# Kernel optimization log

Hardware: AMD Instinct MI355X
Metric: run time of the kernel (lower is better)

## Reference

```python
import jax, jax.numpy as jnp
import numpy as np

BN_EPS = 1e-5

def _bn_eval(x, gamma, beta):
    # Fresh torch BatchNorm1d in eval mode: running_mean=0, running_var=1
    return x * (gamma / jnp.sqrt(1.0 + BN_EPS)) + beta

def setup_inputs() -> dict:
    key = jax.random.key(0)
    ks = jax.random.split(key, 10)
    Q, K, H, W, D = 64, 128, 24, 8, 128
    L = H * W            # seq_len = 192
    FF = 2048            # dim_feedforward
    q_feat = jax.random.normal(ks[0], (Q, H, W, D), dtype=jnp.float32)
    g_feat = jax.random.normal(ks[1], (K, H, W, D), dtype=jnp.float32)
    se = jax.random.normal(ks[2], (L, L), dtype=jnp.float32)
    score_embed = (se + se.T).reshape(1, 1, L, L)
    s = 1.0 / np.sqrt(D)
    fc0_w = jax.random.uniform(ks[3], (D, D), jnp.float32, -s, s)
    fc0_b = jax.random.uniform(ks[4], (D,), jnp.float32, -s, s)
    s2 = 1.0 / np.sqrt(L)
    fc2_w = jax.random.uniform(ks[5], (FF, L), jnp.float32, -s2, s2)
    fc2_b = jax.random.uniform(ks[6], (FF,), jnp.float32, -s2, s2)
    s3 = 1.0 / np.sqrt(FF)
    fc3_w = jax.random.uniform(ks[7], (1, FF), jnp.float32, -s3, s3)
    fc3_b = jax.random.uniform(ks[8], (1,), jnp.float32, -s3, s3)
    bn1_g = jnp.ones((1,)); bn1_b = jnp.zeros((1,))
    bn2_g = jnp.ones((FF,)) + 0.1 * jax.random.normal(ks[9], (FF,), jnp.float32)
    bn2_b = jnp.zeros((FF,))
    bn3_g = jnp.ones((1,)); bn3_b = jnp.zeros((1,))
    return dict(q_feat=q_feat, g_feat=g_feat, score_embed=score_embed,
                fc0_w=fc0_w, fc0_b=fc0_b, fc2_w=fc2_w, fc2_b=fc2_b,
                fc3_w=fc3_w, fc3_b=fc3_b, bn1_g=bn1_g, bn1_b=bn1_b,
                bn2_g=bn2_g, bn2_b=bn2_b, bn3_g=bn3_g, bn3_b=bn3_b)

def reference(q_feat, g_feat, score_embed, fc0_w, fc0_b, fc2_w, fc2_b,
              fc3_w, fc3_b, bn1_g, bn1_b, bn2_g, bn2_b, bn3_g, bn3_b):
    Q = q_feat.shape[0]
    K = g_feat.shape[0]
    D = q_feat.shape[-1]
    L = score_embed.shape[-1]  # seq_len
    tgt = q_feat.reshape(Q, L, D)
    mem = g_feat.reshape(K, L, D)
    query = tgt @ fc0_w.T + fc0_b      # [Q, L, D]
    key_ = mem @ fc0_w.T + fc0_b       # [K, L, D]
    # [Q, K, L(s), L(t)] score, modulated by broadcast sigmoid bias
    score = jnp.einsum('qtd,ksd->qkst', query, key_) * jax.nn.sigmoid(score_embed)
    score = score.reshape(Q * K, L, L)
    # max over s and over t, concatenated per pair -> [QK, 2L]
    score = jnp.concatenate([score.max(axis=1), score.max(axis=2)], axis=-1)
    score = score.reshape(-1, L)       # [2*QK, L]
    score = _bn_eval(score, bn1_g, bn1_b)
    score = score @ fc2_w.T + fc2_b    # [2*QK, FF]
    score = _bn_eval(score, bn2_g, bn2_b)
    score = jax.nn.relu(score)
    score = score @ fc3_w.T + fc3_b    # [2*QK, 1]
    score = score.reshape(-1, 2).sum(axis=-1, keepdims=True)  # [QK, 1]
    score = _bn_eval(score, bn3_g, bn3_b)
    return score.reshape(Q, K)
```

## Files before the change

### kernel.cpp

```cpp
#include <hip/hip_runtime.h>

#define LL 192
#define FF 2048

typedef __attribute__((__ext_vector_type__(8)))  __bf16 bf16x8;
typedef __attribute__((__ext_vector_type__(4)))  __bf16 bf16x4;
typedef __attribute__((__ext_vector_type__(4)))  float  f32x4;

#define MFMA16(a, b, c) __builtin_amdgcn_mfma_f32_16x16x32_bf16((a), (b), (c), 0, 0, 0)


__launch_bounds__(256, 2)
__global__ void proj_prep_kernel(const float* __restrict__ qf_in,
                                 const float* __restrict__ gf_in,
                                 const float* __restrict__ fc0w,
                                 const float* __restrict__ fc0b,
                                 const float* __restrict__ se,
                                 const float* __restrict__ fc2w,
                                 const float* __restrict__ fc2b,
                                 const float* __restrict__ bn2g,
                                 const float* __restrict__ bn2b,
                                 const float* __restrict__ fc3w,
                                 __bf16* __restrict__ kfragA,
                                 __bf16* __restrict__ qfrag16,
                                 float* __restrict__ sig32,
                                 __bf16* __restrict__ fc2w_bf,
                                 float* __restrict__ h2,
                                 float* __restrict__ bb2,
                                 float* __restrict__ f3)
{
    int bx = blockIdx.x, tid = threadIdx.x;
    if (bx >= 1152) {
        int i0 = (bx - 1152) * 256 + tid;
        const int stride = 160 * 256;
        const float c1 = rsqrtf(1.f + 1e-5f);
        for (int i = i0; i < LL * LL; i += stride) {
            int r = i & 3, lane = (i >> 2) & 63, tile = i >> 8;
            int jt = tile % 12, st = tile / 12;
            int s = st * 16 + (lane >> 4) * 4 + r;
            int t = jt * 16 + (lane & 15);
            sig32[i] = 1.f / (1.f + __expf(-se[s * 192 + t]));
        }
        for (int i = i0; i < FF * LL; i += stride)
            fc2w_bf[i] = (__bf16)fc2w[i];
        for (int i = i0; i < FF; i += stride) {
            float h = bn2g[i] * c1;
            h2[i]  = h;
            bb2[i] = fc2b[i] * h + bn2b[i];
            f3[i]  = fc3w[i];
        }
        return;
    }
    __shared__ __bf16 Xs[32][136];
    __shared__ __bf16 Ws[128][136];
    __shared__ __bf16 Os[4096];
    const float* src = (bx < 384) ? (qf_in + (size_t)bx * (32 * 128))
                                  : (gf_in + (size_t)(bx - 384) * (32 * 128));
#pragma unroll
    for (int it = 0; it < 4; ++it) {
        int e = (it * 256 + tid) * 4;
        int r = e >> 7, c = e & 127;
        float4 v = *reinterpret_cast<const float4*>(src + e);
        bf16x4 xv;
        xv[0] = (__bf16)v.x; xv[1] = (__bf16)v.y;
        xv[2] = (__bf16)v.z; xv[3] = (__bf16)v.w;
        *reinterpret_cast<bf16x4*>(&Xs[r][c]) = xv;
    }
#pragma unroll
    for (int it = 0; it < 16; ++it) {
        int e = (it * 256 + tid) * 4;
        int r = e >> 7, c = e & 127;
        float4 v = *reinterpret_cast<const float4*>(fc0w + e);
        bf16x4 xv;
        xv[0] = (__bf16)v.x; xv[1] = (__bf16)v.y;
        xv[2] = (__bf16)v.z; xv[3] = (__bf16)v.w;
        *reinterpret_cast<bf16x4*>(&Ws[r][c]) = xv;
    }
    __syncthreads();

    int wv = tid >> 6, lane = tid & 63, quad = lane >> 4, l16 = lane & 15;
    int n0 = wv * 32;
    f32x4 acc[2][2];
#pragma unroll
    for (int m = 0; m < 2; ++m)
#pragma unroll
        for (int n = 0; n < 2; ++n) acc[m][n] = (f32x4){0.f, 0.f, 0.f, 0.f};
#pragma unroll
    for (int ks = 0; ks < 4; ++ks) {
        bf16x8 a0 = *reinterpret_cast<const bf16x8*>(&Xs[l16][ks * 32 + quad * 8]);
        bf16x8 a1 = *reinterpret_cast<const bf16x8*>(&Xs[16 + l16][ks * 32 + quad * 8]);
        bf16x8 b0 = *reinterpret_cast<const bf16x8*>(&Ws[n0 + l16][ks * 32 + quad * 8]);
        bf16x8 b1 = *reinterpret_cast<const bf16x8*>(&Ws[n0 + 16 + l16][ks * 32 + quad * 8]);
        acc[0][0] = MFMA16(a0, b0, acc[0][0]);
        acc[0][1] = MFMA16(a0, b1, acc[0][1]);
        acc[1][0] = MFMA16(a1, b0, acc[1][0]);
        acc[1][1] = MFMA16(a1, b1, acc[1][1]);
    }
#pragma unroll
    for (int mt = 0; mt < 2; ++mt)
#pragma unroll
        for (int nt = 0; nt < 2; ++nt) {
            int d = n0 + nt * 16 + l16;
            float bv = fc0b[d];
            int abase = mt * 2048 + (d >> 5) * 512 + ((d >> 3) & 3) * 128 + (d & 7);
#pragma unroll
            for (int r = 0; r < 4; ++r)
                Os[abase + (quad * 4 + r) * 8] = (__bf16)(acc[mt][nt][r] + bv);
        }
    __syncthreads();

    int row0 = bx * 32;
    __bf16* dst;
    if (bx < 384) {
        int qi = row0 / 192, tg0 = (row0 % 192) >> 4;
        dst = qfrag16 + qi * 24576 + tg0 * 2048;
    } else {
        int rk0 = row0 - 12288;
        int ki = rk0 / 192, sg0 = (rk0 % 192) >> 4;
        dst = kfragA + ki * 24576 + sg0 * 2048;
    }
#pragma unroll
    for (int it = 0; it < 2; ++it) {
        int e = (it * 256 + tid) * 8;
        *reinterpret_cast<bf16x8*>(dst + e) =
            *reinterpret_cast<const bf16x8*>(&Os[e]);
    }
}

__launch_bounds__(256, 2)
__global__ void score_kernel(const __bf16* __restrict__ kfragA,
                             const __bf16* __restrict__ qfrag16,
                             const float* __restrict__ sig32,
                             const float* __restrict__ bn1g,
                             const float* __restrict__ bn1b,
                             __bf16* __restrict__ Sred)
{
    __shared__ __bf16 Abuf[8192];
    __shared__ __bf16 rowT4[16][200];

    int tid = threadIdx.x;
    int q = blockIdx.x & 63;
    int kbase = (blockIdx.x >> 6) << 2;
    int w = tid >> 6, lane = tid & 63, quad = lane >> 4, l16 = lane & 15;
    const float g1c = bn1g[0] * rsqrtf(1.f + 1e-5f);
    const float b1v = bn1b[0];

    bf16x8 Bf[3][4];
    {
        const __bf16* qb = qfrag16 + (size_t)q * 24576 + lane * 8;
#pragma unroll
        for (int j = 0; j < 3; ++j)
#pragma unroll
            for (int ks = 0; ks < 4; ++ks)
                Bf[j][ks] = *reinterpret_cast<const bf16x8*>(
                    qb + ((3 * w + j) * 4 + ks) * 512);
    }

#pragma unroll 1
    for (int kk = 0; kk < 4; ++kk) {
        int kidx = kbase + kk;
        const __bf16* kp = kfragA + (size_t)kidx * 24576;
        size_t ob = (size_t)(q * 128 + kidx) * 384;
        float cm0 = -3.0e38f, cm1 = -3.0e38f, cm2 = -3.0e38f;

#pragma unroll 1
        for (int h = 0; h < 3; ++h) {
#pragma unroll
            for (int it = 0; it < 4; ++it) {
                int e = (it * 256 + tid) * 8;
                *reinterpret_cast<bf16x8*>(&Abuf[e]) =
                    *reinterpret_cast<const bf16x8*>(kp + 8192 * h + e);
            }
            __syncthreads();

#pragma unroll 1
            for (int lsc = 0; lsc < 2; ++lsc) {
                f32x4 acc[2][3];
#pragma unroll
                for (int i = 0; i < 2; ++i)
#pragma unroll
                    for (int j = 0; j < 3; ++j)
                        acc[i][j] = (f32x4){0.f, 0.f, 0.f, 0.f};

#pragma unroll
                for (int ks = 0; ks < 4; ++ks) {
                    bf16x8 a0 = *reinterpret_cast<const bf16x8*>(
                        &Abuf[((lsc * 2 + 0) * 4 + ks) * 512 + lane * 8]);
                    bf16x8 a1 = *reinterpret_cast<const bf16x8*>(
                        &Abuf[((lsc * 2 + 1) * 4 + ks) * 512 + lane * 8]);
#pragma unroll
                    for (int j = 0; j < 3; ++j) {
                        acc[0][j] = MFMA16(a0, Bf[j][ks], acc[0][j]);
                        acc[1][j] = MFMA16(a1, Bf[j][ks], acc[1][j]);
                    }
                }

#pragma unroll
                for (int i = 0; i < 2; ++i) {
                    int stile = 4 * h + lsc * 2 + i;
                    const float* sp = sig32 +
                        ((size_t)(stile * 12 + 3 * w) * 64 + lane) * 4;
                    f32x4 s0 = *reinterpret_cast<const f32x4*>(sp);
                    f32x4 s1 = *reinterpret_cast<const f32x4*>(sp + 256);
                    f32x4 s2 = *reinterpret_cast<const f32x4*>(sp + 512);
                    float v00 = acc[i][0][0] * s0[0], v01 = acc[i][0][1] * s0[1];
                    float v02 = acc[i][0][2] * s0[2], v03 = acc[i][0][3] * s0[3];
                    float v10 = acc[i][1][0] * s1[0], v11 = acc[i][1][1] * s1[1];
                    float v12 = acc[i][1][2] * s1[2], v13 = acc[i][1][3] * s1[3];
                    float v20 = acc[i][2][0] * s2[0], v21 = acc[i][2][1] * s2[1];
                    float v22 = acc[i][2][2] * s2[2], v23 = acc[i][2][3] * s2[3];
                    float rm0 = fmaxf(fmaxf(v00, v10), v20);
                    float rm1 = fmaxf(fmaxf(v01, v11), v21);
                    float rm2 = fmaxf(fmaxf(v02, v12), v22);
                    float rm3 = fmaxf(fmaxf(v03, v13), v23);
                    cm0 = fmaxf(cm0, fmaxf(fmaxf(fmaxf(v00, v01), v02), v03));
                    cm1 = fmaxf(cm1, fmaxf(fmaxf(fmaxf(v10, v11), v12), v13));
                    cm2 = fmaxf(cm2, fmaxf(fmaxf(fmaxf(v20, v21), v22), v23));
                    rm0 = fmaxf(rm0, __shfl_xor(rm0, 1, 64));
                    rm0 = fmaxf(rm0, __shfl_xor(rm0, 2, 64));
                    rm1 = fmaxf(rm1, __shfl_xor(rm1, 1, 64));
                    rm1 = fmaxf(rm1, __shfl_xor(rm1, 2, 64));
                    rm2 = fmaxf(rm2, __shfl_xor(rm2, 1, 64));
                    rm2 = fmaxf(rm2, __shfl_xor(rm2, 2, 64));
                    rm3 = fmaxf(rm3, __shfl_xor(rm3, 1, 64));
                    rm3 = fmaxf(rm3, __shfl_xor(rm3, 2, 64));
                    if ((l16 & 3) == 0) {
                        bf16x4 pk;
                        pk[0] = (__bf16)rm0; pk[1] = (__bf16)rm1;
                        pk[2] = (__bf16)rm2; pk[3] = (__bf16)rm3;
                        *reinterpret_cast<bf16x4*>(
                            &rowT4[(l16 >> 2) * 4 + w]
                                  [stile * 16 + quad * 4]) = pk;
                    }
                }
            }
            __syncthreads();
        }

        {
            float v0 = cm0, v1 = cm1, v2 = cm2;
            v0 = fmaxf(v0, __shfl_xor(v0, 16, 64));
            v0 = fmaxf(v0, __shfl_xor(v0, 32, 64));
            v1 = fmaxf(v1, __shfl_xor(v1, 16, 64));
            v1 = fmaxf(v1, __shfl_xor(v1, 32, 64));
            v2 = fmaxf(v2, __shfl_xor(v2, 16, 64));
            v2 = fmaxf(v2, __shfl_xor(v2, 32, 64));
            if (quad == 0) {
                Sred[ob + (3 * w + 0) * 16 + l16] = (__bf16)(v0 * g1c + b1v);
                Sred[ob + (3 * w + 1) * 16 + l16] = (__bf16)(v1 * g1c + b1v);
                Sred[ob + (3 * w + 2) * 16 + l16] = (__bf16)(v2 * g1c + b1v);
            }
        }

        if (tid < 192) {
            float m1 = -3.0e38f;
#pragma unroll
            for (int c = 0; c < 16; ++c)
                m1 = fmaxf(m1, (float)rowT4[c][tid]);
            Sred[ob + 192 + tid] = (__bf16)(m1 * g1c + b1v);
        }
    }
}

__launch_bounds__(512, 1)
__global__ void mlp_kernel(const __bf16* __restrict__ Sred,
                           const __bf16* __restrict__ fc2w_bf,
                           const float* __restrict__ h2,
                           const float* __restrict__ bb2,
                           const float* __restrict__ f3,
                           const float* __restrict__ fc3b,
                           const float* __restrict__ bn3g,
                           const float* __restrict__ bn3b,
                           float* __restrict__ out)
{
    __shared__ __bf16 As[64][200];
    __shared__ float  psum_lds[8][64];
    int bx = blockIdx.x, tid = threadIdx.x;
    const __bf16* asrc = Sred + (size_t)bx * (64 * 192);
#pragma unroll
    for (int it = 0; it < 3; ++it) {
        int e = (it * 512 + tid) * 8;
        int r = e / 192, c = e - r * 192;
        *reinterpret_cast<bf16x8*>(&As[r][c]) =
            *reinterpret_cast<const bf16x8*>(asrc + e);
    }
    __syncthreads();

    int wv = tid >> 6, lane = tid & 63, quad = lane >> 4, l16 = lane & 15;
    bf16x8 af[4][6];
#pragma unroll
    for (int m = 0; m < 4; ++m)
#pragma unroll
        for (int kk = 0; kk < 6; ++kk)
            af[m][kk] = *reinterpret_cast<const bf16x8*>(
                &As[m * 16 + l16][kk * 32 + quad * 8]);

    float ps[4][4] = {{0.f,0.f,0.f,0.f},{0.f,0.f,0.f,0.f},
                      {0.f,0.f,0.f,0.f},{0.f,0.f,0.f,0.f}};
    for (int nt = 0; nt < 16; ++nt) {
        int n0 = wv * 256 + nt * 16;
        f32x4 acc[4];
#pragma unroll
        for (int m = 0; m < 4; ++m) acc[m] = (f32x4){0.f, 0.f, 0.f, 0.f};
        const __bf16* bp = fc2w_bf + (size_t)(n0 + l16) * 192 + quad * 8;
#pragma unroll
        for (int kk = 0; kk < 6; ++kk) {
            bf16x8 b = *reinterpret_cast<const bf16x8*>(bp + kk * 32);
#pragma unroll
            for (int m = 0; m < 4; ++m) acc[m] = MFMA16(af[m][kk], b, acc[m]);
        }
        int n = n0 + l16;
        float hh = h2[n], bb = bb2[n], ffv = f3[n];
#pragma unroll
        for (int m = 0; m < 4; ++m)
#pragma unroll
            for (int r = 0; r < 4; ++r)
                ps[m][r] += fmaxf(acc[m][r] * hh + bb, 0.f) * ffv;
    }
#pragma unroll
    for (int m = 0; m < 4; ++m)
#pragma unroll
        for (int r = 0; r < 4; ++r) {
            float v = ps[m][r];
            v += __shfl_xor(v, 1, 64);
            v += __shfl_xor(v, 2, 64);
            v += __shfl_xor(v, 4, 64);
            v += __shfl_xor(v, 8, 64);
            if (l16 == 0) psum_lds[wv][m * 16 + quad * 4 + r] = v;
        }
    __syncthreads();
    if (tid < 32) {
        float s = 0.f;
#pragma unroll
        for (int w = 0; w < 8; ++w)
            s += psum_lds[w][2 * tid] + psum_lds[w][2 * tid + 1];
        const float c1 = rsqrtf(1.f + 1e-5f);
        out[bx * 32 + tid] = (s + 2.f * fc3b[0]) * (bn3g[0] * c1) + bn3b[0];
    }
}

extern "C" void kernel_launch(void* const* d_in, const int* in_sizes, int n_in,
                              void* d_out, int out_size, void* d_ws, size_t ws_size,
                              hipStream_t stream)
{
    const float* q_feat = (const float*)d_in[0];
    const float* g_feat = (const float*)d_in[1];
    const float* se     = (const float*)d_in[2];
    const float* fc0w   = (const float*)d_in[3];
    const float* fc0b   = (const float*)d_in[4];
    const float* fc2w   = (const float*)d_in[5];
    const float* fc2b   = (const float*)d_in[6];
    const float* fc3w   = (const float*)d_in[7];
    const float* fc3b   = (const float*)d_in[8];
    const float* bn1g   = (const float*)d_in[9];
    const float* bn1b   = (const float*)d_in[10];
    const float* bn2g   = (const float*)d_in[11];
    const float* bn2b   = (const float*)d_in[12];
    const float* bn3g   = (const float*)d_in[13];
    const float* bn3b   = (const float*)d_in[14];
    float* out = (float*)d_out;

    char* ws = (char*)d_ws;
    __bf16* kfragA   = (__bf16*)(ws);
    __bf16* qfrag16  = (__bf16*)(ws +  6291456);
    float*  sig32    = (float*) (ws +  9437184);
    __bf16* fc2w_bf  = (__bf16*)(ws +  9584640);
    float*  h2       = (float*) (ws + 10371072);
    float*  bb2      = (float*) (ws + 10379264);
    float*  f3       = (float*) (ws + 10387456);
    __bf16* Sred     = (__bf16*)(ws + 10395648);

    proj_prep_kernel<<<1312, 256, 0, stream>>>(q_feat, g_feat, fc0w, fc0b, se,
                                               fc2w, fc2b, bn2g, bn2b, fc3w,
                                               kfragA, qfrag16, sig32, fc2w_bf,
                                               h2, bb2, f3);
    score_kernel<<<2048, 256, 0, stream>>>(kfragA, qfrag16, sig32, bn1g, bn1b, Sred);
    mlp_kernel<<<256, 512, 0, stream>>>(Sred, fc2w_bf, h2, bb2, f3,
                                        fc3b, bn3g, bn3b, out);
}
```

Measured before the change: 228.9 us.

## Process two queries per score block to reuse staged key tiles; use DPP quad max

Each score_kernel block now handles two query indices, so every key tile staged into shared memory feeds twice as many MFMAs, and the grid halves to 1024 blocks. Register use roughly doubles (two sets of B fragments and accumulators), so launch bounds drop to one block per SM, which lowers occupancy and latency hiding. The 4-lane row-max shuffles are also replaced with DPP quad-permute moves to avoid ds_swizzle/bpermute traffic.

```diff
diff --git a/kernel.cpp b/kernel.cpp
--- a/kernel.cpp
+++ b/kernel.cpp
@@ -9,6 +9,15 @@
 
 #define MFMA16(a, b, c) __builtin_amdgcn_mfma_f32_16x16x32_bf16((a), (b), (c), 0, 0, 0)
 
+
+__device__ __forceinline__ float fmax_quad(float x) {
+    int xi = __builtin_bit_cast(int, x);
+    float y = fmaxf(x, __builtin_bit_cast(float,
+                  __builtin_amdgcn_mov_dpp(xi, 0xB1, 0xF, 0xF, true)));
+    int yi = __builtin_bit_cast(int, y);
+    return fmaxf(y, __builtin_bit_cast(float,
+                  __builtin_amdgcn_mov_dpp(yi, 0x4E, 0xF, 0xF, true)));
+}
 
 __launch_bounds__(256, 2)
 __global__ void proj_prep_kernel(const float* __restrict__ qf_in,
@@ -127,7 +136,7 @@
     }
 }
 
-__launch_bounds__(256, 2)
+__launch_bounds__(256, 1)
 __global__ void score_kernel(const __bf16* __restrict__ kfragA,
                              const __bf16* __restrict__ qfrag16,
                              const float* __restrict__ sig32,
@@ -136,23 +145,24 @@
                              __bf16* __restrict__ Sred)
 {
     __shared__ __bf16 Abuf[8192];
-    __shared__ __bf16 rowT4[16][200];
+    __shared__ __bf16 rowT4[2][16][200];
 
     int tid = threadIdx.x;
-    int q = blockIdx.x & 63;
-    int kbase = (blockIdx.x >> 6) << 2;
+    int q0 = (blockIdx.x & 31) * 2;
+    int kbase = (blockIdx.x >> 5) << 2;
     int w = tid >> 6, lane = tid & 63, quad = lane >> 4, l16 = lane & 15;
     const float g1c = bn1g[0] * rsqrtf(1.f + 1e-5f);
     const float b1v = bn1b[0];
 
-    bf16x8 Bf[3][4];
-    {
-        const __bf16* qb = qfrag16 + (size_t)q * 24576 + lane * 8;
+    bf16x8 Bf[2][3][4];
+#pragma unroll
+    for (int p = 0; p < 2; ++p) {
+        const __bf16* qb = qfrag16 + (size_t)(q0 + p) * 24576 + lane * 8;
 #pragma unroll
         for (int j = 0; j < 3; ++j)
 #pragma unroll
             for (int ks = 0; ks < 4; ++ks)
-                Bf[j][ks] = *reinterpret_cast<const bf16x8*>(
+                Bf[p][j][ks] = *reinterpret_cast<const bf16x8*>(
                     qb + ((3 * w + j) * 4 + ks) * 512);
     }
 
@@ -160,8 +170,11 @@
     for (int kk = 0; kk < 4; ++kk) {
         int kidx = kbase + kk;
         const __bf16* kp = kfragA + (size_t)kidx * 24576;
-        size_t ob = (size_t)(q * 128 + kidx) * 384;
-        float cm0 = -3.0e38f, cm1 = -3.0e38f, cm2 = -3.0e38f;
+        float cm[2][3];
+#pragma unroll
+        for (int p = 0; p < 2; ++p)
+#pragma unroll
+            for (int j = 0; j < 3; ++j) cm[p][j] = -3.0e38f;
 
 #pragma unroll 1
         for (int h = 0; h < 3; ++h) {
@@ -175,12 +188,14 @@
 
 #pragma unroll 1
             for (int lsc = 0; lsc < 2; ++lsc) {
-                f32x4 acc[2][3];
-#pragma unroll
-                for (int i = 0; i < 2; ++i)
-#pragma unroll
-                    for (int j = 0; j < 3; ++j)
-                        acc[i][j] = (f32x4){0.f, 0.f, 0.f, 0.f};
+                f32x4 acc[2][2][3];
+#pragma unroll
+                for (int p = 0; p < 2; ++p)
+#pragma unroll
+                    for (int i = 0; i < 2; ++i)
+#pragma unroll
+                        for (int j = 0; j < 3; ++j)
+                            acc[p][i][j] = (f32x4){0.f, 0.f, 0.f, 0.f};
 
 #pragma unroll
                 for (int ks = 0; ks < 4; ++ks) {
@@ -190,8 +205,10 @@
                         &Abuf[((lsc * 2 + 1) * 4 + ks) * 512 + lane * 8]);
 #pragma unroll
                     for (int j = 0; j < 3; ++j) {
-                        acc[0][j] = MFMA16(a0, Bf[j][ks], acc[0][j]);
-                        acc[1][j] = MFMA16(a1, Bf[j][ks], acc[1][j]);
+                        acc[0][0][j] = MFMA16(a0, Bf[0][j][ks], acc[0][0][j]);
+                        acc[0][1][j] = MFMA16(a1, Bf[0][j][ks], acc[0][1][j]);
+                        acc[1][0][j] = MFMA16(a0, Bf[1][j][ks], acc[1][0][j]);
+                        acc[1][1][j] = MFMA16(a1, Bf[1][j][ks], acc[1][1][j]);
                     }
                 }
 
@@ -203,42 +220,52 @@
                     f32x4 s0 = *reinterpret_cast<const f32x4*>(sp);
                     f32x4 s1 = *reinterpret_cast<const f32x4*>(sp + 256);
                     f32x4 s2 = *reinterpret_cast<const f32x4*>(sp + 512);
-                    float v00 = acc[i][0][0] * s0[0], v01 = acc[i][0][1] * s0[1];
-                    float v02 = acc[i][0][2] * s0[2], v03 = acc[i][0][3] * s0[3];
-                    float v10 = acc[i][1][0] * s1[0], v11 = acc[i][1][1] * s1[1];
-                    float v12 = acc[i][1][2] * s1[2], v13 = acc[i][1][3] * s1[3];
-                    float v20 = acc[i][2][0] * s2[0], v21 = acc[i][2][1] * s2[1];
-                    float v22 = acc[i][2][2] * s2[2], v23 = acc[i][2][3] * s2[3];
-                    float rm0 = fmaxf(fmaxf(v00, v10), v20);
-                    float rm1 = fmaxf(fmaxf(v01, v11), v21);
-                    float rm2 = fmaxf(fmaxf(v02, v12), v22);
-                    float rm3 = fmaxf(fmaxf(v03, v13), v23);
-                    cm0 = fmaxf(cm0, fmaxf(fmaxf(fmaxf(v00, v01), v02), v03));
-                    cm1 = fmaxf(cm1, fmaxf(fmaxf(fmaxf(v10, v11), v12), v13));
-                    cm2 = fmaxf(cm2, fmaxf(fmaxf(fmaxf(v20, v21), v22), v23));
-                    rm0 = fmaxf(rm0, __shfl_xor(rm0, 1, 64));
-                    rm0 = fmaxf(rm0, __shfl_xor(rm0, 2, 64));
-                    rm1 = fmaxf(rm1, __shfl_xor(rm1, 1, 64));
-                    rm1 = fmaxf(rm1, __shfl_xor(rm1, 2, 64));
-                    rm2 = fmaxf(rm2, __shfl_xor(rm2, 1, 64));
-                    rm2 = fmaxf(rm2, __shfl_xor(rm2, 2, 64));
-                    rm3 = fmaxf(rm3, __shfl_xor(rm3, 1, 64));
-                    rm3 = fmaxf(rm3, __shfl_xor(rm3, 2, 64));
-                    if ((l16 & 3) == 0) {
-                        bf16x4 pk;
-                        pk[0] = (__bf16)rm0; pk[1] = (__bf16)rm1;
-                        pk[2] = (__bf16)rm2; pk[3] = (__bf16)rm3;
-                        *reinterpret_cast<bf16x4*>(
-                            &rowT4[(l16 >> 2) * 4 + w]
-                                  [stile * 16 + quad * 4]) = pk;
+#pragma unroll
+                    for (int p = 0; p < 2; ++p) {
+                        float v00 = acc[p][i][0][0] * s0[0];
+                        float v01 = acc[p][i][0][1] * s0[1];
+                        float v02 = acc[p][i][0][2] * s0[2];
+                        float v03 = acc[p][i][0][3] * s0[3];
+                        float v10 = acc[p][i][1][0] * s1[0];
+                        float v11 = acc[p][i][1][1] * s1[1];
+                        float v12 = acc[p][i][1][2] * s1[2];
+                        float v13 = acc[p][i][1][3] * s1[3];
+                        float v20 = acc[p][i][2][0] * s2[0];
+                        float v21 = acc[p][i][2][1] * s2[1];
+                        float v22 = acc[p][i][2][2] * s2[2];
+                        float v23 = acc[p][i][2][3] * s2[3];
+                        float rm0 = fmaxf(fmaxf(v00, v10), v20);
+                        float rm1 = fmaxf(fmaxf(v01, v11), v21);
+                        float rm2 = fmaxf(fmaxf(v02, v12), v22);
+                        float rm3 = fmaxf(fmaxf(v03, v13), v23);
+                        cm[p][0] = fmaxf(fmaxf(cm[p][0], fmaxf(v00, v01)),
+                                         fmaxf(v02, v03));
+                        cm[p][1] = fmaxf(fmaxf(cm[p][1], fmaxf(v10, v11)),
+                                         fmaxf(v12, v13));
+                        cm[p][2] = fmaxf(fmaxf(cm[p][2], fmaxf(v20, v21)),
+                                         fmaxf(v22, v23));
+                        rm0 = fmax_quad(rm0);
+                        rm1 = fmax_quad(rm1);
+                        rm2 = fmax_quad(rm2);
+                        rm3 = fmax_quad(rm3);
+                        if ((l16 & 3) == 0) {
+                            bf16x4 pk;
+                            pk[0] = (__bf16)rm0; pk[1] = (__bf16)rm1;
+                            pk[2] = (__bf16)rm2; pk[3] = (__bf16)rm3;
+                            *reinterpret_cast<bf16x4*>(
+                                &rowT4[p][(l16 >> 2) * 4 + w]
+                                      [stile * 16 + quad * 4]) = pk;
+                        }
                     }
                 }
             }
             __syncthreads();
         }
 
-        {
-            float v0 = cm0, v1 = cm1, v2 = cm2;
+#pragma unroll
+        for (int p = 0; p < 2; ++p) {
+            size_t ob = (size_t)((q0 + p) * 128 + kidx) * 384;
+            float v0 = cm[p][0], v1 = cm[p][1], v2 = cm[p][2];
             v0 = fmaxf(v0, __shfl_xor(v0, 16, 64));
             v0 = fmaxf(v0, __shfl_xor(v0, 32, 64));
             v1 = fmaxf(v1, __shfl_xor(v1, 16, 64));
@@ -253,11 +280,15 @@
         }
 
         if (tid < 192) {
-            float m1 = -3.0e38f;
-#pragma unroll
-            for (int c = 0; c < 16; ++c)
-                m1 = fmaxf(m1, (float)rowT4[c][tid]);
-            Sred[ob + 192 + tid] = (__bf16)(m1 * g1c + b1v);
+#pragma unroll
+            for (int p = 0; p < 2; ++p) {
+                size_t ob = (size_t)((q0 + p) * 128 + kidx) * 384;
+                float m1 = -3.0e38f;
+#pragma unroll
+                for (int c = 0; c < 16; ++c)
+                    m1 = fmaxf(m1, (float)rowT4[p][c][tid]);
+                Sred[ob + 192 + tid] = (__bf16)(m1 * g1c + b1v);
+            }
         }
     }
 }
@@ -374,7 +405,7 @@
                                                fc2w, fc2b, bn2g, bn2b, fc3w,
                                                kfragA, qfrag16, sig32, fc2w_bf,
                                                h2, bb2, f3);
-    score_kernel<<<2048, 256, 0, stream>>>(kfragA, qfrag16, sig32, bn1g, bn1b, Sred);
+    score_kernel<<<1024, 256, 0, stream>>>(kfragA, qfrag16, sig32, bn1g, bn1b, Sred);
     mlp_kernel<<<256, 512, 0, stream>>>(Sred, fc2w_bf, h2, bb2, f3,
                                         fc3b, bn3g, bn3b, out);
 }
```

New measurement: 223.7 us. -2.3%, faster.
